# Optimization experiments

Measured on AMD Instinct MI355X. Metric: run time of the kernel, lower is better.

Reference implementation:

```python
import jax, jax.numpy as jnp
import numpy as np

B, T, D, H = 512, 128, 128, 256


def _uniform(key, shape, fan):
    s = 1.0 / np.sqrt(fan)
    return jax.random.uniform(key, shape, minval=-s, maxval=s, dtype=jnp.float32)


def setup_inputs() -> dict:
    key = jax.random.key(0)
    ks = jax.random.split(key, 16)
    return {
        "x": jax.random.normal(ks[0], (B, T, D), jnp.float32),
        "mask": jax.random.randint(ks[1], (B, T, D), 0, 2).astype(jnp.int32),
        # nn.LSTMCell(2D, H): weights init U(-1/sqrt(H), 1/sqrt(H))
        "W_ih": _uniform(ks[2], (4 * H, 2 * D), H),
        "W_hh": _uniform(ks[3], (4 * H, H), H),
        "b_ih": _uniform(ks[4], (4 * H,), H),
        "b_hh": _uniform(ks[5], (4 * H,), H),
        # TemporalDecay h: W [H, D], stdv = 1/sqrt(W.size(0)) = 1/sqrt(H)
        "W_dh": _uniform(ks[6], (H, D), H),
        "b_dh": _uniform(ks[7], (H,), H),
        # TemporalDecay x (diag): W [D, D]
        "W_dx": _uniform(ks[8], (D, D), D),
        "b_dx": _uniform(ks[9], (D,), D),
        # hist_reg Linear(H, D): torch default U(-1/sqrt(H), 1/sqrt(H))
        "W_hr": _uniform(ks[10], (D, H), H),
        "b_hr": _uniform(ks[11], (D,), H),
        "W_fr": _uniform(ks[12], (D, D), D),
        "b_fr": _uniform(ks[13], (D,), D),
        # weight_combine Linear(2D, D)
        "W_wc": _uniform(ks[14], (D, 2 * D), 2 * D),
        "b_wc": _uniform(ks[15], (D,), 2 * D),
    }


def _compute_delta(m_tm):
    # m_tm: [T, B, D] float; delta[0]=0, delta[t]=m[t-1] + (1-m[t-1])*(delta[t-1]+1)
    Tn, Bn, Dn = m_tm.shape
    def step(prev, m_prev):
        new = m_prev + (1.0 - m_prev) * (prev + 1.0)
        return new, new
    _, rest = jax.lax.scan(step, jnp.zeros((Bn, Dn), m_tm.dtype), m_tm[:-1])
    return jnp.concatenate([jnp.zeros((1, Bn, Dn), m_tm.dtype), rest], axis=0)


def _rits_forward(x, mask, W_ih, W_hh, b_ih, b_hh, W_dh, b_dh, W_dx, b_dx,
                  W_hr, b_hr, W_fr, b_fr, W_wc, b_wc):
    Bn, Tn, Dn = x.shape
    Hn = W_hh.shape[1]
    m = mask.astype(x.dtype)
    x_tm = jnp.swapaxes(x, 0, 1)   # [T,B,D]
    m_tm = jnp.swapaxes(m, 0, 1)   # [T,B,D]
    deltas = _compute_delta(m_tm)  # [T,B,D]

    W_fr_masked = W_fr * (1.0 - jnp.eye(Dn, dtype=x.dtype))  # zero diagonal
    dx_diag = jnp.diag(W_dx)  # diag-masked linear == elementwise scale

    def step(carry, inputs):
        h, c = carry
        xt, mt, dt = inputs
        gamma_h = jnp.exp(-jax.nn.relu(dt @ W_dh.T + b_dh))      # [B,H]
        gamma_x = jnp.exp(-jax.nn.relu(dt * dx_diag + b_dx))     # [B,D]
        h = h * gamma_h
        x_h = h @ W_hr.T + b_hr                                  # [B,D]
        x_c = jnp.where(mt > 0, xt, x_h)
        z_h = x_c @ W_fr_masked.T + b_fr                         # [B,D]
        alpha = jnp.concatenate([gamma_x, mt], axis=1) @ W_wc.T + b_wc
        c_h = alpha * z_h + (1.0 - alpha) * x_h
        c_c = jnp.where(mt > 0, xt, c_h)
        lstm_in = jnp.concatenate([c_c, mt], axis=1)             # [B,2D]
        gates = lstm_in @ W_ih.T + b_ih + h @ W_hh.T + b_hh      # [B,4H]
        i, f, g, o = jnp.split(gates, 4, axis=1)
        c_new = jax.nn.sigmoid(f) * c + jax.nn.sigmoid(i) * jnp.tanh(g)
        h_new = jax.nn.sigmoid(o) * jnp.tanh(c_new)
        return (h_new, c_new), (x_h, z_h, c_h)

    init = (jnp.zeros((Bn, Hn), x.dtype), jnp.zeros((Bn, Hn), x.dtype))
    _, (first, second, third) = jax.lax.scan(step, init, (x_tm, m_tm, deltas))
    first = jnp.swapaxes(first, 0, 1)
    second = jnp.swapaxes(second, 0, 1)
    third = jnp.swapaxes(third, 0, 1)
    return first, second, third, third  # x_out == third (both are c_h)


def reference(x, mask, W_ih, W_hh, b_ih, b_hh, W_dh, b_dh, W_dx, b_dx,
              W_hr, b_hr, W_fr, b_fr, W_wc, b_wc):
    return _rits_forward(x, mask, W_ih, W_hh, b_ih, b_hh, W_dh, b_dh,
                         W_dx, b_dx, W_hr, b_hr, W_fr, b_fr, W_wc, b_wc)
```

## Files before the change

### kernel.cpp

```cpp
#include <hip/hip_runtime.h>

typedef unsigned short u16;
typedef unsigned int u32;
typedef unsigned long long u64;
typedef __attribute__((ext_vector_type(8))) short s16x8;
typedef __attribute__((ext_vector_type(4))) float f32x4;

#define MFMA16(a, b, c) __builtin_amdgcn_mfma_f32_16x16x32_bf16((a), (b), (c), 0, 0, 0)

static constexpr int Bn = 512, Tn = 128, Dn = 128, Hn = 256;
static constexpr int NG = 4 * Hn;
static constexpr int KG = 2 * Dn + Hn;
static constexpr long long BTD = (long long)Bn * Tn * Dn;

__device__ __forceinline__ u16 f2bf(float f) {
  union { float f; unsigned u; } v; v.f = f;
  unsigned u = v.u;
  return (u16)((u + 0x7fffu + ((u >> 16) & 1u)) >> 16);
}
__device__ __forceinline__ float bf2f(u16 h) {
  union { unsigned u; float f; } v; v.u = ((unsigned)h) << 16;
  return v.f;
}
__device__ __forceinline__ float sigm(float x) {
  return __builtin_amdgcn_rcpf(1.f + __expf(-x));
}
__device__ __forceinline__ float ftanh(float x) {
  return 1.f - 2.f * __builtin_amdgcn_rcpf(1.f + __expf(2.f * x));
}

__global__ void k_pack(const float* __restrict__ W_ih, const float* __restrict__ W_hh,
                       const float* __restrict__ W_hr, const float* __restrict__ W_fr,
                       const float* __restrict__ W_dh, const float* __restrict__ W_wc,
                       u16* Wg, u16* Whr_b, u16* Wfr_b, u16* Wdh_b, u16* Wwc_b) {
  int i = blockIdx.x * 256 + threadIdx.x;
  if (i < NG * KG) {
    int n = i >> 9, k = i & 511;
    float v = (k < 256) ? W_ih[n * 256 + k] : W_hh[n * 256 + (k - 256)];
    Wg[i] = f2bf(v);
  }
  if (i < Dn * Hn) Whr_b[i] = f2bf(W_hr[i]);
  if (i < Dn * Dn) {
    int r = i >> 7, c = i & 127;
    Wfr_b[i] = f2bf(r == c ? 0.f : W_fr[i]);
  }
  if (i < Hn * Dn) Wdh_b[i] = f2bf(W_dh[i]);
  if (i < Dn * Hn) Wwc_b[i] = f2bf(W_wc[i]);
}

__global__ void k_delta(const float* __restrict__ x, const int* __restrict__ mask,
                        const float* __restrict__ W_dx, const float* __restrict__ b_dx,
                        u16* delta_bf, u16* gx_bf, u16* m_bf, u16* x_bf) {
  int idx = blockIdx.x * 256 + threadIdx.x;
  int b = idx >> 7, d = idx & 127;
  float dxd = W_dx[d * Dn + d], bxd = b_dx[d];
  float del = 0.f;
  for (int t = 0; t < Tn; ++t) {
    long long o = ((long long)t * Bn + b) * Dn + d;
    long long gi = ((long long)b * Tn + t) * Dn + d;
    delta_bf[o] = f2bf(del);
    gx_bf[o] = f2bf(expf(-fmaxf(del * dxd + bxd, 0.f)));
    float m = (float)mask[gi];
    m_bf[o] = f2bf(m);
    x_bf[o] = f2bf(x[gi]);
    del = m + (1.f - m) * (del + 1.f);
  }
}

__global__ void k_gammah(const u16* __restrict__ delta_bf, const u16* __restrict__ Wdh_b,
                         const float* __restrict__ b_dh, u16* __restrict__ gammah) {
  int bid = blockIdx.x;
  int t = bid >> 5, b0 = (bid & 31) << 4;
  int tid = threadIdx.x, wid = tid >> 6, l = tid & 63;
  int lr = l & 15, lg = l >> 4;
  const u16* Arow = delta_bf + ((long long)t * Bn + b0) * Dn;
  s16x8 afr[4];
#pragma unroll
  for (int ks = 0; ks < 4; ++ks)
    afr[ks] = *(const s16x8*)(Arow + (long long)lr * Dn + ks * 32 + lg * 8);
#pragma unroll
  for (int q = 0; q < 4; ++q) {
    int n0 = (wid * 4 + q) * 16;
    f32x4 acc = {0.f, 0.f, 0.f, 0.f};
#pragma unroll
    for (int ks = 0; ks < 4; ++ks) {
      s16x8 bfr = *(const s16x8*)(Wdh_b + (long long)(n0 + lr) * Dn + ks * 32 + lg * 8);
      acc = MFMA16(afr[ks], bfr, acc);
    }
    int n = n0 + lr;
    float bb = b_dh[n];
#pragma unroll
    for (int r = 0; r < 4; ++r) {
      int row = lg * 4 + r;
      float g = expf(-fmaxf(acc[r] + bb, 0.f));
      gammah[((long long)t * Bn + b0 + row) * Hn + n] = f2bf(g);
    }
  }
}

__global__ void k_alpha(const u16* __restrict__ gx_bf, const u16* __restrict__ m_bf,
                        const u16* __restrict__ Wwc_b, const float* __restrict__ b_wc,
                        u16* __restrict__ alpha) {
  int bid = blockIdx.x;
  int t = bid >> 5, b0 = (bid & 31) << 4;
  int tid = threadIdx.x, wid = tid >> 6, l = tid & 63;
  int lr = l & 15, lg = l >> 4;
  s16x8 afr[8];
#pragma unroll
  for (int ks = 0; ks < 8; ++ks) {
    const u16* src = (ks < 4) ? gx_bf : m_bf;
    int kk = (ks & 3) * 32 + lg * 8;
    afr[ks] = *(const s16x8*)(src + ((long long)t * Bn + b0 + lr) * Dn + kk);
  }
#pragma unroll
  for (int q = 0; q < 2; ++q) {
    int n0 = (wid * 2 + q) * 16;
    f32x4 acc = {0.f, 0.f, 0.f, 0.f};
#pragma unroll
    for (int ks = 0; ks < 8; ++ks) {
      s16x8 bfr = *(const s16x8*)(Wwc_b + (long long)(n0 + lr) * (2 * Dn) + ks * 32 + lg * 8);
      acc = MFMA16(afr[ks], bfr, acc);
    }
    int n = n0 + lr;
    float bb = b_wc[n];
#pragma unroll
    for (int r = 0; r < 4; ++r)
      alpha[((long long)t * Bn + b0 + lg * 4 + r) * Dn + n] = f2bf(acc[r] + bb);
  }
}

__global__ __launch_bounds__(512) void k_main(
    const u16* __restrict__ x_bf, const u16* __restrict__ m_bf,
    const u16* __restrict__ Wg, const u16* __restrict__ Whr_b, const u16* __restrict__ Wfr_b,
    const u16* __restrict__ gammah, const u16* __restrict__ alpha,
    const float* __restrict__ b_ih, const float* __restrict__ b_hh,
    const float* __restrict__ b_hr, const float* __restrict__ b_fr,
    float* __restrict__ out, u64* __restrict__ Hex, int* __restrict__ cnt) {
  __shared__ __align__(16) u16 A_lds[64 * 128];
  __shared__ __align__(16) u16 Axc[16 * 128];
  __shared__ __align__(16) float G_lds[16 * 128];

  const int tid = threadIdx.x, wid = tid >> 6, l = tid & 63;
  const int lr = l & 15, lg = l >> 4;
  const int g = blockIdx.x & 31, s = blockIdx.x >> 5;
  const int b0 = g * 16;
  int* const cntg = cnt + g * 64;

  for (int i = tid; i < 32 * 128; i += 512) A_lds[32 * 128 + i] = 0;

  const int dd = wid * 16 + lr;
  const float bhr = b_hr[dd], bfr = b_fr[dd];

  const int prow = tid >> 5, pjj = tid & 31;
  const int pj = 32 * s + pjj;
  const float bg0 = b_ih[0 * 256 + pj] + b_hh[0 * 256 + pj];
  const float bg1 = b_ih[1 * 256 + pj] + b_hh[1 * 256 + pj];
  const float bg2 = b_ih[2 * 256 + pj] + b_hh[2 * 256 + pj];
  const float bg3 = b_ih[3 * 256 + pj] + b_hh[3 * 256 + pj];

  s16x8 whr[8], wfr[4], wg[16];
#pragma unroll
  for (int ks = 0; ks < 8; ++ks)
    whr[ks] = *(const s16x8*)(Whr_b + (long long)dd * Hn + ks * 32 + lg * 8);
#pragma unroll
  for (int ks = 0; ks < 4; ++ks)
    wfr[ks] = *(const s16x8*)(Wfr_b + (long long)dd * Dn + ks * 32 + lg * 8);
  {
    const int q = wid >> 1;
    const long long grow = q * 256 + 32 * s + 16 * (wid & 1) + lr;
#pragma unroll
    for (int ks = 0; ks < 16; ++ks)
      wg[ks] = *(const s16x8*)(Wg + grow * KG + ks * 32 + lg * 8);
  }

  const u16* a_base = A_lds + lg * 128 + lr * 8;
  const u16* axc_base = Axc + lg * 128 + lr * 8;

  float cst = 0.f;
  float xn[4], mnv[4], an[4];
#pragma unroll
  for (int r = 0; r < 4; ++r) {
    int row = lg * 4 + r;
    long long o = ((long long)0 * Bn + b0 + row) * Dn + dd;
    xn[r] = bf2f(x_bf[o]); mnv[r] = bf2f(m_bf[o]); an[r] = bf2f(alpha[o]);
  }

  float* out0 = out;
  float* out1 = out + BTD;
  float* out2 = out + 2 * BTD;
  float* out3 = out + 3 * BTD;

#pragma unroll 1
  for (int t = 0; t < Tn; ++t) {
    __syncthreads();
    float gmh = 1.f;
    if (t + 1 < Tn)
      gmh = bf2f(gammah[((long long)(t + 1) * Bn + b0 + prow) * Hn + pj]);

    f32x4 acc = {0.f, 0.f, 0.f, 0.f};
#pragma unroll
    for (int ks = 0; ks < 8; ++ks) {
      s16x8 a = *(const s16x8*)(a_base + 32 * 128 + ks * 512);
      acc = MFMA16(a, whr[ks], acc);
    }
    float xh[4], xv[4], av[4], mv[4];
#pragma unroll
    for (int r = 0; r < 4; ++r) {
      int row = lg * 4 + r;
      xh[r] = acc[r] + bhr;
      xv[r] = xn[r]; mv[r] = mnv[r]; av[r] = an[r];
      float xc = (mv[r] > 0.5f) ? xv[r] : xh[r];
      Axc[(dd >> 3) * 128 + row * 8 + (dd & 7)] = f2bf(xc);
      A_lds[(16 + (dd >> 3)) * 128 + row * 8 + (dd & 7)] = f2bf(mv[r]);
    }
    __syncthreads();

    acc = f32x4{0.f, 0.f, 0.f, 0.f};
#pragma unroll
    for (int ks = 0; ks < 4; ++ks) {
      s16x8 a = *(const s16x8*)(axc_base + ks * 512);
      acc = MFMA16(a, wfr[ks], acc);
    }
    float zv[4], chv[4];
#pragma unroll
    for (int r = 0; r < 4; ++r) {
      int row = lg * 4 + r;
      zv[r] = acc[r] + bfr;
      chv[r] = av[r] * zv[r] + (1.f - av[r]) * xh[r];
      float ccv = (mv[r] > 0.5f) ? xv[r] : chv[r];
      A_lds[(dd >> 3) * 128 + row * 8 + (dd & 7)] = f2bf(ccv);
    }
    __syncthreads();

    if (t + 1 < Tn) {
#pragma unroll
      for (int r = 0; r < 4; ++r) {
        int row = lg * 4 + r;
        long long o = ((long long)(t + 1) * Bn + b0 + row) * Dn + dd;
        xn[r] = bf2f(x_bf[o]); mnv[r] = bf2f(m_bf[o]); an[r] = bf2f(alpha[o]);
      }
    }
    acc = f32x4{0.f, 0.f, 0.f, 0.f};
#pragma unroll
    for (int ks = 0; ks < 16; ++ks) {
      s16x8 a = *(const s16x8*)(a_base + ks * 512);
      acc = MFMA16(a, wg[ks], acc);
    }
#pragma unroll
    for (int r = 0; r < 4; ++r)
      G_lds[(lg * 4 + r) * 128 + wid * 16 + lr] = acc[r];
    __syncthreads();

    float gi = G_lds[prow * 128 + 0 * 32 + pjj] + bg0;
    float gf = G_lds[prow * 128 + 1 * 32 + pjj] + bg1;
    float gg = G_lds[prow * 128 + 2 * 32 + pjj] + bg2;
    float go = G_lds[prow * 128 + 3 * 32 + pjj] + bg3;
    float iv = sigm(gi), fv = sigm(gf), gv = ftanh(gg), ov = sigm(go);
    cst = fv * cst + iv * gv;
    float h = ov * ftanh(cst);

    if (t + 1 < Tn) {
      unsigned hv = (unsigned)f2bf(h * gmh);
      unsigned up = (unsigned)__shfl_xor((int)hv, 1);
      u32* HexW = (u32*)(Hex + (size_t)((t + 1) & 1) * 32768 + (size_t)g * 1024);
      if (!(tid & 1))
        __hip_atomic_store(HexW + (prow * 128 + (pj >> 1)), hv | (up << 16),
                           __ATOMIC_RELAXED, __HIP_MEMORY_SCOPE_AGENT);
      __syncthreads();
      if (tid == 0)
        __hip_atomic_fetch_add(cntg, 1, __ATOMIC_RELAXED, __HIP_MEMORY_SCOPE_AGENT);
    }

    if (wid == s) {
#pragma unroll
      for (int r = 0; r < 4; ++r) {
        int row = lg * 4 + r;
        long long gx = ((long long)(b0 + row) * Tn + t) * Dn + dd;
        out0[gx] = xh[r];
        out1[gx] = zv[r];
        out2[gx] = chv[r];
        out3[gx] = chv[r];
      }
    }

    if (t + 1 < Tn) {
      const int target = 8 * (t + 1);
      for (;;) {
        int v = __hip_atomic_load(cntg, __ATOMIC_RELAXED, __HIP_MEMORY_SCOPE_AGENT);
        if (v >= target) break;
      }
      const u64* HexR = Hex + (size_t)((t + 1) & 1) * 32768 + (size_t)g * 1024;
      int row = tid & 15, c = tid >> 4;
      u64 w0 = __hip_atomic_load(HexR + row * 64 + c * 2,
                                 __ATOMIC_RELAXED, __HIP_MEMORY_SCOPE_AGENT);
      u64 w1 = __hip_atomic_load(HexR + row * 64 + c * 2 + 1,
                                 __ATOMIC_RELAXED, __HIP_MEMORY_SCOPE_AGENT);
      u64* dst = (u64*)(A_lds + (32 + c) * 128 + row * 8);
      dst[0] = w0; dst[1] = w1;
    }
  }
}

extern "C" void kernel_launch(void* const* d_in, const int* in_sizes, int n_in,
                              void* d_out, int out_size, void* d_ws, size_t ws_size,
                              hipStream_t stream) {
  (void)in_sizes; (void)n_in; (void)out_size; (void)ws_size;
  const float* x = (const float*)d_in[0];
  const int* mask = (const int*)d_in[1];
  const float* W_ih = (const float*)d_in[2];
  const float* W_hh = (const float*)d_in[3];
  const float* b_ih = (const float*)d_in[4];
  const float* b_hh = (const float*)d_in[5];
  const float* W_dh = (const float*)d_in[6];
  const float* b_dh = (const float*)d_in[7];
  const float* W_dx = (const float*)d_in[8];
  const float* b_dx = (const float*)d_in[9];
  const float* W_hr = (const float*)d_in[10];
  const float* b_hr = (const float*)d_in[11];
  const float* W_fr = (const float*)d_in[12];
  const float* b_fr = (const float*)d_in[13];
  const float* W_wc = (const float*)d_in[14];
  const float* b_wc = (const float*)d_in[15];

  char* ws = (char*)d_ws;
  size_t off = 0;
  auto alloc = [&](size_t bytes) {
    void* p = ws + off;
    off = (off + bytes + 255) & ~(size_t)255;
    return p;
  };
  const long long TBD = (long long)Tn * Bn * Dn;
  const long long TBH = (long long)Tn * Bn * Hn;
  u16* delta_bf = (u16*)alloc(TBD * 2);
  u16* gx_bf    = (u16*)alloc(TBD * 2);
  u16* m_bf     = (u16*)alloc(TBD * 2);
  u16* x_bf     = (u16*)alloc(TBD * 2);
  u16* gammah   = (u16*)alloc(TBH * 2);
  u16* alphaw   = (u16*)alloc(TBD * 2);
  u16* Wg    = (u16*)alloc((size_t)NG * KG * 2);
  u16* Whr_b = (u16*)alloc((size_t)Dn * Hn * 2);
  u16* Wfr_b = (u16*)alloc((size_t)Dn * Dn * 2);
  u16* Wdh_b = (u16*)alloc((size_t)Hn * Dn * 2);
  u16* Wwc_b = (u16*)alloc((size_t)Dn * Hn * 2);

  u64* Hex = (u64*)delta_bf;
  int* cnt = (int*)((char*)delta_bf + 512 * 1024);

  k_pack<<<2048, 256, 0, stream>>>(W_ih, W_hh, W_hr, W_fr, W_dh, W_wc,
                                   Wg, Whr_b, Wfr_b, Wdh_b, Wwc_b);
  k_delta<<<(Bn * Dn) / 256, 256, 0, stream>>>(x, mask, W_dx, b_dx,
                                               delta_bf, gx_bf, m_bf, x_bf);
  k_gammah<<<Tn * (Bn / 16), 256, 0, stream>>>(delta_bf, Wdh_b, b_dh, gammah);
  k_alpha<<<Tn * (Bn / 16), 256, 0, stream>>>(gx_bf, m_bf, Wwc_b, b_wc, alphaw);
  hipMemsetAsync(cnt, 0, 32 * 256, stream);

  void* args[] = {
    (void*)&x_bf, (void*)&m_bf, (void*)&Wg, (void*)&Whr_b, (void*)&Wfr_b,
    (void*)&gammah, (void*)&alphaw, (void*)&b_ih, (void*)&b_hh,
    (void*)&b_hr, (void*)&b_fr, (void*)&d_out, (void*)&Hex, (void*)&cnt
  };
  hipLaunchCooperativeKernel((const void*)k_main, dim3(256), dim3(512), args, 0, stream);
}
```

Measured before the change: 593.4 us.

## Replace per-step counter barrier with per-wave flags and merge precompute kernels

The per-step cross-block handshake in the recurrent kernel no longer uses a block-wide __syncthreads plus an atomic counter increment. Each wave now waits on its own stores and then publishes a step-number flag, and readers poll all 64 flags of their group with a wave-wide vote. The gamma_h and alpha precompute kernels are merged into one launch, k_delta batches its x/mask loads four steps at a time, and expf is replaced by __expf. This is meant to shorten the serial critical path per timestep and remove launch overhead, at the cost of more polling traffic and slightly lower exp accuracy.

```diff
diff --git a/kernel.cpp b/kernel.cpp
--- a/kernel.cpp
+++ b/kernel.cpp
@@ -55,77 +55,87 @@
   int b = idx >> 7, d = idx & 127;
   float dxd = W_dx[d * Dn + d], bxd = b_dx[d];
   float del = 0.f;
-  for (int t = 0; t < Tn; ++t) {
-    long long o = ((long long)t * Bn + b) * Dn + d;
-    long long gi = ((long long)b * Tn + t) * Dn + d;
-    delta_bf[o] = f2bf(del);
-    gx_bf[o] = f2bf(expf(-fmaxf(del * dxd + bxd, 0.f)));
-    float m = (float)mask[gi];
-    m_bf[o] = f2bf(m);
-    x_bf[o] = f2bf(x[gi]);
-    del = m + (1.f - m) * (del + 1.f);
-  }
-}
-
-__global__ void k_gammah(const u16* __restrict__ delta_bf, const u16* __restrict__ Wdh_b,
-                         const float* __restrict__ b_dh, u16* __restrict__ gammah) {
-  int bid = blockIdx.x;
-  int t = bid >> 5, b0 = (bid & 31) << 4;
+  const float* xrow = x + (long long)b * Tn * Dn + d;
+  const int* mrow = mask + (long long)b * Tn * Dn + d;
+  for (int t0 = 0; t0 < Tn; t0 += 4) {
+    float xv[4]; int mv[4];
+#pragma unroll
+    for (int k = 0; k < 4; ++k) {
+      xv[k] = xrow[(t0 + k) * Dn];
+      mv[k] = mrow[(t0 + k) * Dn];
+    }
+#pragma unroll
+    for (int k = 0; k < 4; ++k) {
+      int t = t0 + k;
+      long long o = ((long long)t * Bn + b) * Dn + d;
+      delta_bf[o] = f2bf(del);
+      gx_bf[o] = f2bf(__expf(-fmaxf(del * dxd + bxd, 0.f)));
+      float m = (float)mv[k];
+      m_bf[o] = f2bf(m);
+      x_bf[o] = f2bf(xv[k]);
+      del = m + (1.f - m) * (del + 1.f);
+    }
+  }
+}
+
+__global__ void k_ga(const u16* __restrict__ delta_bf, const u16* __restrict__ gx_bf,
+                     const u16* __restrict__ m_bf,
+                     const u16* __restrict__ Wdh_b, const u16* __restrict__ Wwc_b,
+                     const float* __restrict__ b_dh, const float* __restrict__ b_wc,
+                     u16* __restrict__ gammah, u16* __restrict__ alpha) {
   int tid = threadIdx.x, wid = tid >> 6, l = tid & 63;
   int lr = l & 15, lg = l >> 4;
-  const u16* Arow = delta_bf + ((long long)t * Bn + b0) * Dn;
-  s16x8 afr[4];
-#pragma unroll
-  for (int ks = 0; ks < 4; ++ks)
-    afr[ks] = *(const s16x8*)(Arow + (long long)lr * Dn + ks * 32 + lg * 8);
-#pragma unroll
-  for (int q = 0; q < 4; ++q) {
-    int n0 = (wid * 4 + q) * 16;
-    f32x4 acc = {0.f, 0.f, 0.f, 0.f};
-#pragma unroll
-    for (int ks = 0; ks < 4; ++ks) {
-      s16x8 bfr = *(const s16x8*)(Wdh_b + (long long)(n0 + lr) * Dn + ks * 32 + lg * 8);
-      acc = MFMA16(afr[ks], bfr, acc);
-    }
-    int n = n0 + lr;
-    float bb = b_dh[n];
-#pragma unroll
-    for (int r = 0; r < 4; ++r) {
-      int row = lg * 4 + r;
-      float g = expf(-fmaxf(acc[r] + bb, 0.f));
-      gammah[((long long)t * Bn + b0 + row) * Hn + n] = f2bf(g);
-    }
-  }
-}
-
-__global__ void k_alpha(const u16* __restrict__ gx_bf, const u16* __restrict__ m_bf,
-                        const u16* __restrict__ Wwc_b, const float* __restrict__ b_wc,
-                        u16* __restrict__ alpha) {
-  int bid = blockIdx.x;
-  int t = bid >> 5, b0 = (bid & 31) << 4;
-  int tid = threadIdx.x, wid = tid >> 6, l = tid & 63;
-  int lr = l & 15, lg = l >> 4;
-  s16x8 afr[8];
-#pragma unroll
-  for (int ks = 0; ks < 8; ++ks) {
-    const u16* src = (ks < 4) ? gx_bf : m_bf;
-    int kk = (ks & 3) * 32 + lg * 8;
-    afr[ks] = *(const s16x8*)(src + ((long long)t * Bn + b0 + lr) * Dn + kk);
-  }
-#pragma unroll
-  for (int q = 0; q < 2; ++q) {
-    int n0 = (wid * 2 + q) * 16;
-    f32x4 acc = {0.f, 0.f, 0.f, 0.f};
+  if (blockIdx.x < 4096) {
+    int bid = blockIdx.x;
+    int t = bid >> 5, b0 = (bid & 31) << 4;
+    const u16* Arow = delta_bf + ((long long)t * Bn + b0) * Dn;
+    s16x8 afr[4];
+#pragma unroll
+    for (int ks = 0; ks < 4; ++ks)
+      afr[ks] = *(const s16x8*)(Arow + (long long)lr * Dn + ks * 32 + lg * 8);
+#pragma unroll
+    for (int q = 0; q < 4; ++q) {
+      int n0 = (wid * 4 + q) * 16;
+      f32x4 acc = {0.f, 0.f, 0.f, 0.f};
+#pragma unroll
+      for (int ks = 0; ks < 4; ++ks) {
+        s16x8 bfr = *(const s16x8*)(Wdh_b + (long long)(n0 + lr) * Dn + ks * 32 + lg * 8);
+        acc = MFMA16(afr[ks], bfr, acc);
+      }
+      int n = n0 + lr;
+      float bb = b_dh[n];
+#pragma unroll
+      for (int r = 0; r < 4; ++r) {
+        int row = lg * 4 + r;
+        float g = __expf(-fmaxf(acc[r] + bb, 0.f));
+        gammah[((long long)t * Bn + b0 + row) * Hn + n] = f2bf(g);
+      }
+    }
+  } else {
+    int bid = blockIdx.x - 4096;
+    int t = bid >> 5, b0 = (bid & 31) << 4;
+    s16x8 afr[8];
 #pragma unroll
     for (int ks = 0; ks < 8; ++ks) {
-      s16x8 bfr = *(const s16x8*)(Wwc_b + (long long)(n0 + lr) * (2 * Dn) + ks * 32 + lg * 8);
-      acc = MFMA16(afr[ks], bfr, acc);
-    }
-    int n = n0 + lr;
-    float bb = b_wc[n];
-#pragma unroll
-    for (int r = 0; r < 4; ++r)
-      alpha[((long long)t * Bn + b0 + lg * 4 + r) * Dn + n] = f2bf(acc[r] + bb);
+      const u16* src = (ks < 4) ? gx_bf : m_bf;
+      int kk = (ks & 3) * 32 + lg * 8;
+      afr[ks] = *(const s16x8*)(src + ((long long)t * Bn + b0 + lr) * Dn + kk);
+    }
+#pragma unroll
+    for (int q = 0; q < 2; ++q) {
+      int n0 = (wid * 2 + q) * 16;
+      f32x4 acc = {0.f, 0.f, 0.f, 0.f};
+#pragma unroll
+      for (int ks = 0; ks < 8; ++ks) {
+        s16x8 bfr = *(const s16x8*)(Wwc_b + (long long)(n0 + lr) * (2 * Dn) + ks * 32 + lg * 8);
+        acc = MFMA16(afr[ks], bfr, acc);
+      }
+      int n = n0 + lr;
+      float bb = b_wc[n];
+#pragma unroll
+      for (int r = 0; r < 4; ++r)
+        alpha[((long long)t * Bn + b0 + lg * 4 + r) * Dn + n] = f2bf(acc[r] + bb);
+    }
   }
 }
 
@@ -135,7 +145,7 @@
     const u16* __restrict__ gammah, const u16* __restrict__ alpha,
     const float* __restrict__ b_ih, const float* __restrict__ b_hh,
     const float* __restrict__ b_hr, const float* __restrict__ b_fr,
-    float* __restrict__ out, u64* __restrict__ Hex, int* __restrict__ cnt) {
+    float* __restrict__ out, u64* __restrict__ Hex, int* __restrict__ flags) {
   __shared__ __align__(16) u16 A_lds[64 * 128];
   __shared__ __align__(16) u16 Axc[16 * 128];
   __shared__ __align__(16) float G_lds[16 * 128];
@@ -144,7 +154,7 @@
   const int lr = l & 15, lg = l >> 4;
   const int g = blockIdx.x & 31, s = blockIdx.x >> 5;
   const int b0 = g * 16;
-  int* const cntg = cnt + g * 64;
+  int* const flg = flags + g * 64;
 
   for (int i = tid; i < 32 * 128; i += 512) A_lds[32 * 128 + i] = 0;
 
@@ -264,11 +274,12 @@
       unsigned up = (unsigned)__shfl_xor((int)hv, 1);
       u32* HexW = (u32*)(Hex + (size_t)((t + 1) & 1) * 32768 + (size_t)g * 1024);
       if (!(tid & 1))
-        __hip_atomic_store(HexW + (prow * 128 + (pj >> 1)), hv | (up << 16),
+        __hip_atomic_store(HexW + (prow * 128 + 16 * s + (pjj >> 1)), hv | (up << 16),
                            __ATOMIC_RELAXED, __HIP_MEMORY_SCOPE_AGENT);
-      __syncthreads();
-      if (tid == 0)
-        __hip_atomic_fetch_add(cntg, 1, __ATOMIC_RELAXED, __HIP_MEMORY_SCOPE_AGENT);
+      asm volatile("s_waitcnt vmcnt(0)" ::: "memory");
+      if (l == 0)
+        __hip_atomic_store(flg + s * 8 + wid, t + 1,
+                           __ATOMIC_RELAXED, __HIP_MEMORY_SCOPE_AGENT);
     }
 
     if (wid == s) {
@@ -284,11 +295,11 @@
     }
 
     if (t + 1 < Tn) {
-      const int target = 8 * (t + 1);
-      for (;;) {
-        int v = __hip_atomic_load(cntg, __ATOMIC_RELAXED, __HIP_MEMORY_SCOPE_AGENT);
-        if (v >= target) break;
-      }
+      const int target = t + 1;
+      int v;
+      do {
+        v = __hip_atomic_load(flg + l, __ATOMIC_RELAXED, __HIP_MEMORY_SCOPE_AGENT);
+      } while (!__all(v >= target));
       const u64* HexR = Hex + (size_t)((t + 1) & 1) * 32768 + (size_t)g * 1024;
       int row = tid & 15, c = tid >> 4;
       u64 w0 = __hip_atomic_load(HexR + row * 64 + c * 2,
@@ -344,20 +355,20 @@
   u16* Wwc_b = (u16*)alloc((size_t)Dn * Hn * 2);
 
   u64* Hex = (u64*)delta_bf;
-  int* cnt = (int*)((char*)delta_bf + 512 * 1024);
+  int* flags = (int*)((char*)delta_bf + 512 * 1024);
 
   k_pack<<<2048, 256, 0, stream>>>(W_ih, W_hh, W_hr, W_fr, W_dh, W_wc,
                                    Wg, Whr_b, Wfr_b, Wdh_b, Wwc_b);
   k_delta<<<(Bn * Dn) / 256, 256, 0, stream>>>(x, mask, W_dx, b_dx,
                                                delta_bf, gx_bf, m_bf, x_bf);
-  k_gammah<<<Tn * (Bn / 16), 256, 0, stream>>>(delta_bf, Wdh_b, b_dh, gammah);
-  k_alpha<<<Tn * (Bn / 16), 256, 0, stream>>>(gx_bf, m_bf, Wwc_b, b_wc, alphaw);
-  hipMemsetAsync(cnt, 0, 32 * 256, stream);
+  k_ga<<<8192, 256, 0, stream>>>(delta_bf, gx_bf, m_bf, Wdh_b, Wwc_b,
+                                 b_dh, b_wc, gammah, alphaw);
+  hipMemsetAsync(flags, 0, 32 * 256, stream);
 
   void* args[] = {
     (void*)&x_bf, (void*)&m_bf, (void*)&Wg, (void*)&Whr_b, (void*)&Wfr_b,
     (void*)&gammah, (void*)&alphaw, (void*)&b_ih, (void*)&b_hh,
-    (void*)&b_hr, (void*)&b_fr, (void*)&d_out, (void*)&Hex, (void*)&cnt
+    (void*)&b_hr, (void*)&b_fr, (void*)&d_out, (void*)&Hex, (void*)&flags
   };
   hipLaunchCooperativeKernel((const void*)k_main, dim3(256), dim3(512), args, 0, stream);
 }
```

Result: slower. 1.146 ms (+93.2%).
